# Performance work log

Hardware: AMD Instinct MI355X
Metric: run time of the kernel (lower is better)

## Reference

```python
import jax, jax.numpy as jnp
import numpy as np

N = 50000      # nodes
E = 800000     # edges (avg degree 16)
DIN = 256
DOUT = 256
EA = 16        # edge_attr_dim
EH = 32        # edge_mlp_hidden
Z = 0.8        # z_ratio
EPS = 1e-5


def _lin_init(k, fin, fout):
    k1, k2 = jax.random.split(k)
    s = 1.0 / np.sqrt(fin)
    W = jax.random.uniform(k1, (fin, fout), jnp.float32, -s, s)
    b = jax.random.uniform(k2, (fout,), jnp.float32, -s, s)
    return W, b


def setup_inputs() -> dict:
    key = jax.random.key(0)
    ks = jax.random.split(key, 12)
    x = jax.random.normal(ks[0], (N, DIN), dtype=jnp.float32)
    edge_index = jax.random.randint(ks[1], (2, E), 0, N, dtype=jnp.int64)
    edge_weight = jax.random.uniform(ks[2], (E,), dtype=jnp.float32)
    mask = jax.random.bernoulli(ks[3], 0.5, (N, 1))
    edge_attr = jax.random.normal(ks[4], (E, EA), dtype=jnp.float32)
    Wt0, bt0 = _lin_init(ks[5], DIN, DOUT)
    Wt1, bt1 = _lin_init(ks[6], DIN, DOUT)
    Wc0, bc0 = _lin_init(ks[7], DIN + DOUT, DOUT)
    Wc1, bc1 = _lin_init(ks[8], DIN + DOUT, DOUT)
    gn_w = jnp.ones((DOUT,), jnp.float32)
    gn_b = jnp.zeros((DOUT,), jnp.float32)
    gn_alpha = jnp.ones((DOUT,), jnp.float32)  # GraphNorm mean_scale
    Wm1, bm1 = _lin_init(ks[9], EA, EH)
    Wm2, bm2 = _lin_init(ks[10], EH, 1)
    return {
        'x': x, 'edge_index': edge_index, 'edge_weight': edge_weight,
        'mask': mask, 'edge_attr': edge_attr,
        'Wt0': Wt0, 'bt0': bt0, 'Wt1': Wt1, 'bt1': bt1,
        'Wc0': Wc0, 'bc0': bc0, 'Wc1': Wc1, 'bc1': bc1,
        'gn_w': gn_w, 'gn_b': gn_b, 'gn_alpha': gn_alpha,
        'Wm1': Wm1, 'bm1': bm1, 'Wm2': Wm2, 'bm2': bm2,
    }


def _mix(m, a1, a0):
    # torch.where(mask, z*x1 + (1-z)*x0, z*x0 + (1-z)*x1)
    return jnp.where(m, Z * a1 + (1.0 - Z) * a0, Z * a0 + (1.0 - Z) * a1)


def reference(x, edge_index, edge_weight, mask, edge_attr,
              Wt0, bt0, Wt1, bt1, Wc0, bc0, Wc1, bc1,
              gn_w, gn_b, gn_alpha, Wm1, bm1, Wm2, bm2):
    n_node = x.shape[0]
    row, col = edge_index[0], edge_index[1]

    # edge MLP (scalar mode): edge_weight <- softplus(MLP(edge_attr))
    h = jax.nn.relu(edge_attr @ Wm1 + bm1)
    ew = jax.nn.softplus((h @ Wm2 + bm2))[:, 0]  # [E]

    # buildAdj with aggr='mean': row-normalized weights
    deg = jax.ops.segment_sum(ew, row, num_segments=n_node)
    deg = jnp.where(deg < 0.5, deg + 1.0, deg)
    w = ew / deg[row]  # [E]

    # dual-branch transform + masked mix
    x1 = jax.nn.relu(x @ Wt1 + bt1)
    x0 = jax.nn.relu(x @ Wt0 + bt0)
    xm = _mix(mask, x1, x0)  # [N, DOUT]

    # sparse adj @ x : gather at col, scatter-add at row
    agg = jax.ops.segment_sum(w[:, None] * xm[col], row, num_segments=n_node)

    # GraphNorm (single graph): x - alpha*mean, normalize by std
    mean = jnp.mean(agg, axis=0)
    out = agg - gn_alpha * mean
    var = jnp.mean(out * out, axis=0)
    out = gn_w * out * jax.lax.rsqrt(var + EPS) + gn_b

    # dropout inactive in eval mode
    xc = jnp.concatenate([out, x], axis=-1)  # [N, DOUT+DIN]
    c1 = xc @ Wc1 + bc1
    c0 = xc @ Wc0 + bc0
    return _mix(mask, c1, c0)
```

## Files before the change

kernel.cpp:

```cpp
#include <hip/hip_runtime.h>

#define NN 50000
#define NE 800000
#define NNP 50176

typedef __attribute__((ext_vector_type(4))) float f32x4;
typedef __bf16 bf16x8 __attribute__((ext_vector_type(8)));

__device__ __forceinline__ float bfu2f(unsigned short u) {
  return __uint_as_float(((unsigned)u) << 16);
}
__device__ __forceinline__ unsigned short f2bf(float f) {
  unsigned u = __float_as_uint(f);
  u += 0x7fffu + ((u >> 16) & 1u);
  return (unsigned short)(u >> 16);
}

__global__ __launch_bounds__(256) void transpose_w(
    const float* __restrict__ W, unsigned short* __restrict__ WT, int K, int N) {
  __shared__ unsigned short T[32 * 40];
  const int t = threadIdx.x;
  const int k0 = blockIdx.x * 32, n0 = blockIdx.y * 32;
  const int kk = t >> 3, nn = (t & 7) * 4;
  f32x4 v = *(const f32x4*)(W + (k0 + kk) * N + n0 + nn);
#pragma unroll
  for (int i = 0; i < 4; i++) T[(nn + i) * 40 + kk] = f2bf(v[i]);
  __syncthreads();
  const int nn2 = t >> 3, kk2 = (t & 7) * 4;
  unsigned short o[4];
#pragma unroll
  for (int i = 0; i < 4; i++) o[i] = T[nn2 * 40 + kk2 + i];
  *(uint2*)(WT + (n0 + nn2) * K + k0 + kk2) = *(const uint2*)o;
}

__global__ __launch_bounds__(256) void count_kernel(
    const int* __restrict__ ei, int* __restrict__ cnt, int* __restrict__ rank) {
  const int e = blockIdx.x * 256 + threadIdx.x;
  if (e >= NE) return;
  rank[e] = atomicAdd(&cnt[ei[e]], 1);
}

__global__ __launch_bounds__(256) void scan1_kernel(const int* __restrict__ cnt,
                                                    int* __restrict__ blockSum) {
  __shared__ int sd[256];
  const int t = threadIdx.x;
  sd[t] = cnt[blockIdx.x * 256 + t];
  __syncthreads();
  for (int off = 128; off > 0; off >>= 1) {
    if (t < off) sd[t] += sd[t + off];
    __syncthreads();
  }
  if (t == 0) blockSum[blockIdx.x] = sd[0];
}

__global__ __launch_bounds__(256) void scan2_kernel(int* __restrict__ blockSum) {
  __shared__ int sd[256];
  const int t = threadIdx.x;
  int v = (t < 196) ? blockSum[t] : 0;
  sd[t] = v;
  __syncthreads();
  for (int off = 1; off < 256; off <<= 1) {
    int y = (t >= off) ? sd[t - off] : 0;
    __syncthreads();
    sd[t] += y;
    __syncthreads();
  }
  int ex = (t == 0) ? 0 : sd[t - 1];
  __syncthreads();
  if (t < 196) blockSum[t] = ex;
}

__global__ __launch_bounds__(256) void scan3_kernel(
    const int* __restrict__ cnt, const int* __restrict__ blockSum,
    int* __restrict__ start) {
  __shared__ int sd[256];
  const int t = threadIdx.x;
  const int row = blockIdx.x * 256 + t;
  const int c = cnt[row];
  sd[t] = c;
  __syncthreads();
  for (int off = 1; off < 256; off <<= 1) {
    int y = (t >= off) ? sd[t - off] : 0;
    __syncthreads();
    sd[t] += y;
    __syncthreads();
  }
  start[row] = blockSum[blockIdx.x] + sd[t] - c;
}

__device__ __forceinline__ void mlp4(float a0, float a1, float a2, float a3,
                                     const f32x4* __restrict__ w,
                                     f32x4& h0, f32x4& h1, f32x4& h2, f32x4& h3,
                                     f32x4& h4, f32x4& h5, f32x4& h6, f32x4& h7) {
  h0 += w[0] * a0;  h1 += w[1] * a0;  h2 += w[2] * a0;  h3 += w[3] * a0;
  h4 += w[4] * a0;  h5 += w[5] * a0;  h6 += w[6] * a0;  h7 += w[7] * a0;
  h0 += w[8] * a1;  h1 += w[9] * a1;  h2 += w[10] * a1; h3 += w[11] * a1;
  h4 += w[12] * a1; h5 += w[13] * a1; h6 += w[14] * a1; h7 += w[15] * a1;
  h0 += w[16] * a2; h1 += w[17] * a2; h2 += w[18] * a2; h3 += w[19] * a2;
  h4 += w[20] * a2; h5 += w[21] * a2; h6 += w[22] * a2; h7 += w[23] * a2;
  h0 += w[24] * a3; h1 += w[25] * a3; h2 += w[26] * a3; h3 += w[27] * a3;
  h4 += w[28] * a3; h5 += w[29] * a3; h6 += w[30] * a3; h7 += w[31] * a3;
}

__device__ __forceinline__ float rdot(f32x4 h, f32x4 w) {
  float s = fmaxf(h[0], 0.0f) * w[0];
  s = fmaf(fmaxf(h[1], 0.0f), w[1], s);
  s = fmaf(fmaxf(h[2], 0.0f), w[2], s);
  s = fmaf(fmaxf(h[3], 0.0f), w[3], s);
  return s;
}

__global__ __launch_bounds__(256) void mlp_fill_kernel(
    const float* __restrict__ ea,
    const float* __restrict__ Wm1, const float* __restrict__ bm1,
    const float* __restrict__ Wm2, const float* __restrict__ bm2,
    const int* __restrict__ ei, const int* __restrict__ start,
    const int* __restrict__ rank, uint2* __restrict__ colw) {
  __shared__ __align__(16) float w1[512];
  __shared__ __align__(16) float b1[32];
  __shared__ __align__(16) float w2[32];
  __shared__ float b2s[1];
  const int t = threadIdx.x;
  w1[t] = Wm1[t];
  w1[t + 256] = Wm1[t + 256];
  if (t < 32) { b1[t] = bm1[t]; w2[t] = Wm2[t]; }
  if (t == 0) b2s[0] = bm2[0];
  __syncthreads();
  const int e = blockIdx.x * 256 + t;
  if (e >= NE) return;
  f32x4 r0 = *(const f32x4*)(ea + e * 16);
  f32x4 r1 = *(const f32x4*)(ea + e * 16 + 4);
  f32x4 r2 = *(const f32x4*)(ea + e * 16 + 8);
  f32x4 r3 = *(const f32x4*)(ea + e * 16 + 12);
  const f32x4* bv = (const f32x4*)b1;
  f32x4 h0 = bv[0], h1 = bv[1], h2 = bv[2], h3 = bv[3];
  f32x4 h4 = bv[4], h5 = bv[5], h6 = bv[6], h7 = bv[7];
  const f32x4* wv = (const f32x4*)w1;
  mlp4(r0[0], r0[1], r0[2], r0[3], wv, h0, h1, h2, h3, h4, h5, h6, h7);
  mlp4(r1[0], r1[1], r1[2], r1[3], wv + 32, h0, h1, h2, h3, h4, h5, h6, h7);
  mlp4(r2[0], r2[1], r2[2], r2[3], wv + 64, h0, h1, h2, h3, h4, h5, h6, h7);
  mlp4(r3[0], r3[1], r3[2], r3[3], wv + 96, h0, h1, h2, h3, h4, h5, h6, h7);
  const f32x4* w2v = (const f32x4*)w2;
  float s = b2s[0];
  s += rdot(h0, w2v[0]) + rdot(h1, w2v[1]) + rdot(h2, w2v[2]) + rdot(h3, w2v[3]);
  s += rdot(h4, w2v[4]) + rdot(h5, w2v[5]) + rdot(h6, w2v[6]) + rdot(h7, w2v[7]);
  const float sp = (s > 0.0f) ? (s + log1pf(expf(-s))) : log1pf(expf(s));
  uint2 p;
  p.x = (unsigned)ei[NE + e];
  p.y = __float_as_uint(sp);
  colw[start[ei[e]] + rank[e]] = p;
}

__global__ __launch_bounds__(256, 2) void gemm_transform(
    const float* __restrict__ X,
    const unsigned short* __restrict__ WT1, const unsigned short* __restrict__ WT0,
    const float* __restrict__ bias1, const float* __restrict__ bias0,
    const int* __restrict__ mask, unsigned short* __restrict__ xmb) {
  __shared__ __align__(16) unsigned short As[128 * 40];
  __shared__ __align__(16) unsigned short Bs1[128 * 40];
  __shared__ __align__(16) unsigned short Bs0[128 * 40];
  const int t = threadIdx.x;
  const int col0 = blockIdx.x * 128, row0 = blockIdx.y * 128;
  const int wv = t >> 6, lane = t & 63, m = lane & 15, q = lane >> 4;
  const int hr = t >> 1, hc = t & 1;
  f32x4 acc1[2][8], acc0[2][8];
#pragma unroll
  for (int rf = 0; rf < 2; rf++)
#pragma unroll
    for (int nt = 0; nt < 8; nt++) { acc1[rf][nt] = (f32x4)(0.0f); acc0[rf][nt] = (f32x4)(0.0f); }
  const int gr = row0 + hr;
  for (int k0 = 0; k0 < 256; k0 += 32) {
    unsigned short av[16];
    if (gr < NN) {
      const float* xp = X + gr * 256 + k0 + hc * 16;
      f32x4 x0 = *(const f32x4*)(xp);
      f32x4 x1 = *(const f32x4*)(xp + 4);
      f32x4 x2 = *(const f32x4*)(xp + 8);
      f32x4 x3 = *(const f32x4*)(xp + 12);
#pragma unroll
      for (int i = 0; i < 4; i++) {
        av[i] = f2bf(x0[i]); av[4 + i] = f2bf(x1[i]);
        av[8 + i] = f2bf(x2[i]); av[12 + i] = f2bf(x3[i]);
      }
    } else {
#pragma unroll
      for (int i = 0; i < 16; i++) av[i] = 0;
    }
    *(uint4*)&As[hr * 40 + hc * 16] = ((const uint4*)av)[0];
    *(uint4*)&As[hr * 40 + hc * 16 + 8] = ((const uint4*)av)[1];
    const unsigned short* w1p = WT1 + (col0 + hr) * 256 + k0 + hc * 16;
    const unsigned short* w0p = WT0 + (col0 + hr) * 256 + k0 + hc * 16;
    uint4 b1a = *(const uint4*)w1p;
    uint4 b1b = *(const uint4*)(w1p + 8);
    uint4 b0a = *(const uint4*)w0p;
    uint4 b0b = *(const uint4*)(w0p + 8);
    *(uint4*)&Bs1[hr * 40 + hc * 16] = b1a;
    *(uint4*)&Bs1[hr * 40 + hc * 16 + 8] = b1b;
    *(uint4*)&Bs0[hr * 40 + hc * 16] = b0a;
    *(uint4*)&Bs0[hr * 40 + hc * 16 + 8] = b0b;
    __syncthreads();
    bf16x8 af[2];
#pragma unroll
    for (int rf = 0; rf < 2; rf++)
      af[rf] = *(const bf16x8*)&As[(wv * 32 + rf * 16 + m) * 40 + q * 8];
#pragma unroll
    for (int nt = 0; nt < 8; nt++) {
      bf16x8 f1 = *(const bf16x8*)&Bs1[(nt * 16 + m) * 40 + q * 8];
      bf16x8 f0 = *(const bf16x8*)&Bs0[(nt * 16 + m) * 40 + q * 8];
      acc1[0][nt] = __builtin_amdgcn_mfma_f32_16x16x32_bf16(af[0], f1, acc1[0][nt], 0, 0, 0);
      acc1[1][nt] = __builtin_amdgcn_mfma_f32_16x16x32_bf16(af[1], f1, acc1[1][nt], 0, 0, 0);
      acc0[0][nt] = __builtin_amdgcn_mfma_f32_16x16x32_bf16(af[0], f0, acc0[0][nt], 0, 0, 0);
      acc0[1][nt] = __builtin_amdgcn_mfma_f32_16x16x32_bf16(af[1], f0, acc0[1][nt], 0, 0, 0);
    }
    __syncthreads();
  }
#pragma unroll
  for (int rf = 0; rf < 2; rf++) {
    const int rbase = row0 + wv * 32 + rf * 16 + q * 4;
    int mk[4];
#pragma unroll
    for (int r = 0; r < 4; r++) mk[r] = (rbase + r < NN) ? mask[rbase + r] : 0;
#pragma unroll
    for (int nt = 0; nt < 8; nt++) {
      const int gc = col0 + nt * 16 + m;
      const float bb1 = bias1[gc];
      const float bb0 = bias0[gc];
#pragma unroll
      for (int r = 0; r < 4; r++) {
        const int grr = rbase + r;
        if (grr < NN) {
          float v1 = fmaxf(acc1[rf][nt][r] + bb1, 0.0f);
          float v0 = fmaxf(acc0[rf][nt][r] + bb0, 0.0f);
          float o = mk[r] ? (0.8f * v1 + 0.2f * v0) : (0.8f * v0 + 0.2f * v1);
          xmb[grr * 256 + gc] = f2bf(o);
        }
      }
    }
  }
}

__global__ __launch_bounds__(256) void aggregate_kernel(
    const int* __restrict__ start, const int* __restrict__ cnt,
    const uint2* __restrict__ colw,
    const unsigned short* __restrict__ xmb, unsigned short* __restrict__ aggb) {
  const int wave = threadIdx.x >> 6, lane = threadIdx.x & 63;
  const int row = blockIdx.x * 4 + wave;
  const int s = start[row];
  const int c = cnt[row];
  const int choff = lane * 4;
  f32x4 acc = (f32x4)(0.0f);
  float dsum = 0.0f;
  int i = 0;
  for (; i + 4 <= c; i += 4) {
    uint2 cw0 = colw[s + i], cw1 = colw[s + i + 1];
    uint2 cw2 = colw[s + i + 2], cw3 = colw[s + i + 3];
    const float w0 = __uint_as_float(cw0.y), w1 = __uint_as_float(cw1.y);
    const float w2 = __uint_as_float(cw2.y), w3 = __uint_as_float(cw3.y);
    uint2 u0 = *(const uint2*)(xmb + (int)cw0.x * 256 + choff);
    uint2 u1 = *(const uint2*)(xmb + (int)cw1.x * 256 + choff);
    uint2 u2 = *(const uint2*)(xmb + (int)cw2.x * 256 + choff);
    uint2 u3 = *(const uint2*)(xmb + (int)cw3.x * 256 + choff);
    dsum += (w0 + w1) + (w2 + w3);
    acc[0] = fmaf(w0, __uint_as_float(u0.x << 16), acc[0]);
    acc[1] = fmaf(w0, __uint_as_float(u0.x & 0xffff0000u), acc[1]);
    acc[2] = fmaf(w0, __uint_as_float(u0.y << 16), acc[2]);
    acc[3] = fmaf(w0, __uint_as_float(u0.y & 0xffff0000u), acc[3]);
    acc[0] = fmaf(w1, __uint_as_float(u1.x << 16), acc[0]);
    acc[1] = fmaf(w1, __uint_as_float(u1.x & 0xffff0000u), acc[1]);
    acc[2] = fmaf(w1, __uint_as_float(u1.y << 16), acc[2]);
    acc[3] = fmaf(w1, __uint_as_float(u1.y & 0xffff0000u), acc[3]);
    acc[0] = fmaf(w2, __uint_as_float(u2.x << 16), acc[0]);
    acc[1] = fmaf(w2, __uint_as_float(u2.x & 0xffff0000u), acc[1]);
    acc[2] = fmaf(w2, __uint_as_float(u2.y << 16), acc[2]);
    acc[3] = fmaf(w2, __uint_as_float(u2.y & 0xffff0000u), acc[3]);
    acc[0] = fmaf(w3, __uint_as_float(u3.x << 16), acc[0]);
    acc[1] = fmaf(w3, __uint_as_float(u3.x & 0xffff0000u), acc[1]);
    acc[2] = fmaf(w3, __uint_as_float(u3.y << 16), acc[2]);
    acc[3] = fmaf(w3, __uint_as_float(u3.y & 0xffff0000u), acc[3]);
  }
  for (; i < c; i++) {
    uint2 cw0 = colw[s + i];
    const float w0 = __uint_as_float(cw0.y);
    uint2 u0 = *(const uint2*)(xmb + (int)cw0.x * 256 + choff);
    dsum += w0;
    acc[0] = fmaf(w0, __uint_as_float(u0.x << 16), acc[0]);
    acc[1] = fmaf(w0, __uint_as_float(u0.x & 0xffff0000u), acc[1]);
    acc[2] = fmaf(w0, __uint_as_float(u0.y << 16), acc[2]);
    acc[3] = fmaf(w0, __uint_as_float(u0.y & 0xffff0000u), acc[3]);
  }
  float d = (dsum < 0.5f) ? dsum + 1.0f : dsum;
  const float inv = 1.0f / d;
  unsigned short o[4];
#pragma unroll
  for (int j = 0; j < 4; j++) o[j] = f2bf(acc[j] * inv);
  *(uint2*)(aggb + row * 256 + choff) = *(const uint2*)o;
}

__global__ __launch_bounds__(256) void stats_kernel(
    const unsigned short* __restrict__ aggb, float* __restrict__ S1, float* __restrict__ S2) {
  const int c = threadIdx.x;
  const int r0 = blockIdx.x * 200;
  float s1 = 0.0f, s2 = 0.0f;
  for (int r = 0; r < 200; r++) {
    float v = bfu2f(aggb[(r0 + r) * 256 + c]);
    s1 += v;
    s2 = fmaf(v, v, s2);
  }
  unsafeAtomicAdd(&S1[c], s1);
  unsafeAtomicAdd(&S2[c], s2);
}

__global__ void finalize_kernel(
    const float* __restrict__ S1, const float* __restrict__ S2,
    const float* __restrict__ gw, const float* __restrict__ gb,
    const float* __restrict__ ga,
    float* __restrict__ scale, float* __restrict__ shift) {
  const int c = threadIdx.x;
  const float inv_n = 1.0f / (float)NN;
  float mean = S1[c] * inv_n;
  float ex2 = S2[c] * inv_n;
  float am = ga[c] * mean;
  float var = ex2 - 2.0f * am * mean + am * am;
  float sc = gw[c] * rsqrtf(var + 1e-5f);
  scale[c] = sc;
  shift[c] = gb[c] - sc * am;
}

__global__ __launch_bounds__(256, 2) void gemm_combine(
    const unsigned short* __restrict__ aggb,
    const float* __restrict__ scale, const float* __restrict__ shift,
    const float* __restrict__ X,
    const unsigned short* __restrict__ WT1, const unsigned short* __restrict__ WT0,
    const float* __restrict__ bias1, const float* __restrict__ bias0,
    const int* __restrict__ mask, float* __restrict__ out) {
  __shared__ __align__(16) unsigned short As[128 * 40];
  __shared__ __align__(16) unsigned short Bs1[128 * 40];
  __shared__ __align__(16) unsigned short Bs0[128 * 40];
  __shared__ float scL[256];
  __shared__ float shL[256];
  const int t = threadIdx.x;
  scL[t] = scale[t];
  shL[t] = shift[t];
  const int col0 = blockIdx.x * 128, row0 = blockIdx.y * 128;
  const int wv = t >> 6, lane = t & 63, m = lane & 15, q = lane >> 4;
  const int hr = t >> 1, hc = t & 1;
  f32x4 acc1[2][8], acc0[2][8];
#pragma unroll
  for (int rf = 0; rf < 2; rf++)
#pragma unroll
    for (int nt = 0; nt < 8; nt++) { acc1[rf][nt] = (f32x4)(0.0f); acc0[rf][nt] = (f32x4)(0.0f); }
  const int gr = row0 + hr;
  __syncthreads();
  for (int k0 = 0; k0 < 512; k0 += 32) {
    unsigned short av[16];
#pragma unroll
    for (int i = 0; i < 16; i++) av[i] = 0;
    if (gr < NN) {
      if (k0 < 256) {
        const int c0 = k0 + hc * 16;
        uint4 ua = *(const uint4*)(aggb + gr * 256 + c0);
        uint4 ub = *(const uint4*)(aggb + gr * 256 + c0 + 8);
        const unsigned short* us = (const unsigned short*)&ua;
        const unsigned short* vs = (const unsigned short*)&ub;
#pragma unroll
        for (int i = 0; i < 8; i++) {
          av[i] = f2bf(fmaf(scL[c0 + i], bfu2f(us[i]), shL[c0 + i]));
          av[8 + i] = f2bf(fmaf(scL[c0 + 8 + i], bfu2f(vs[i]), shL[c0 + 8 + i]));
        }
      } else {
        const float* xp = X + gr * 256 + (k0 - 256) + hc * 16;
        f32x4 x0 = *(const f32x4*)(xp);
        f32x4 x1 = *(const f32x4*)(xp + 4);
        f32x4 x2 = *(const f32x4*)(xp + 8);
        f32x4 x3 = *(const f32x4*)(xp + 12);
#pragma unroll
        for (int i = 0; i < 4; i++) {
          av[i] = f2bf(x0[i]); av[4 + i] = f2bf(x1[i]);
          av[8 + i] = f2bf(x2[i]); av[12 + i] = f2bf(x3[i]);
        }
      }
    }
    *(uint4*)&As[hr * 40 + hc * 16] = ((const uint4*)av)[0];
    *(uint4*)&As[hr * 40 + hc * 16 + 8] = ((const uint4*)av)[1];
    const unsigned short* w1p = WT1 + (col0 + hr) * 512 + k0 + hc * 16;
    const unsigned short* w0p = WT0 + (col0 + hr) * 512 + k0 + hc * 16;
    uint4 b1a = *(const uint4*)w1p;
    uint4 b1b = *(const uint4*)(w1p + 8);
    uint4 b0a = *(const uint4*)w0p;
    uint4 b0b = *(const uint4*)(w0p + 8);
    *(uint4*)&Bs1[hr * 40 + hc * 16] = b1a;
    *(uint4*)&Bs1[hr * 40 + hc * 16 + 8] = b1b;
    *(uint4*)&Bs0[hr * 40 + hc * 16] = b0a;
    *(uint4*)&Bs0[hr * 40 + hc * 16 + 8] = b0b;
    __syncthreads();
    bf16x8 af[2];
#pragma unroll
    for (int rf = 0; rf < 2; rf++)
      af[rf] = *(const bf16x8*)&As[(wv * 32 + rf * 16 + m) * 40 + q * 8];
#pragma unroll
    for (int nt = 0; nt < 8; nt++) {
      bf16x8 f1 = *(const bf16x8*)&Bs1[(nt * 16 + m) * 40 + q * 8];
      bf16x8 f0 = *(const bf16x8*)&Bs0[(nt * 16 + m) * 40 + q * 8];
      acc1[0][nt] = __builtin_amdgcn_mfma_f32_16x16x32_bf16(af[0], f1, acc1[0][nt], 0, 0, 0);
      acc1[1][nt] = __builtin_amdgcn_mfma_f32_16x16x32_bf16(af[1], f1, acc1[1][nt], 0, 0, 0);
      acc0[0][nt] = __builtin_amdgcn_mfma_f32_16x16x32_bf16(af[0], f0, acc0[0][nt], 0, 0, 0);
      acc0[1][nt] = __builtin_amdgcn_mfma_f32_16x16x32_bf16(af[1], f0, acc0[1][nt], 0, 0, 0);
    }
    __syncthreads();
  }
#pragma unroll
  for (int rf = 0; rf < 2; rf++) {
    const int rbase = row0 + wv * 32 + rf * 16 + q * 4;
    int mk[4];
#pragma unroll
    for (int r = 0; r < 4; r++) mk[r] = (rbase + r < NN) ? mask[rbase + r] : 0;
#pragma unroll
    for (int nt = 0; nt < 8; nt++) {
      const int gc = col0 + nt * 16 + m;
      const float bb1 = bias1[gc];
      const float bb0 = bias0[gc];
#pragma unroll
      for (int r = 0; r < 4; r++) {
        const int grr = rbase + r;
        if (grr < NN) {
          float v1 = acc1[rf][nt][r] + bb1;
          float v0 = acc0[rf][nt][r] + bb0;
          float o = mk[r] ? (0.8f * v1 + 0.2f * v0) : (0.8f * v0 + 0.2f * v1);
          out[grr * 256 + gc] = o;
        }
      }
    }
  }
}

extern "C" void kernel_launch(void* const* d_in, const int* in_sizes, int n_in,
                              void* d_out, int out_size, void* d_ws, size_t ws_size,
                              hipStream_t stream) {
  (void)in_sizes; (void)n_in; (void)out_size; (void)ws_size;
  const float* x   = (const float*)d_in[0];
  const int*   ei  = (const int*)d_in[1];
  const int*   msk = (const int*)d_in[3];
  const float* ea  = (const float*)d_in[4];
  const float* Wt0 = (const float*)d_in[5];
  const float* bt0 = (const float*)d_in[6];
  const float* Wt1 = (const float*)d_in[7];
  const float* bt1 = (const float*)d_in[8];
  const float* Wc0 = (const float*)d_in[9];
  const float* bc0 = (const float*)d_in[10];
  const float* Wc1 = (const float*)d_in[11];
  const float* bc1 = (const float*)d_in[12];
  const float* gnw = (const float*)d_in[13];
  const float* gnb = (const float*)d_in[14];
  const float* gna = (const float*)d_in[15];
  const float* Wm1 = (const float*)d_in[16];
  const float* bm1 = (const float*)d_in[17];
  const float* Wm2 = (const float*)d_in[18];
  const float* bm2 = (const float*)d_in[19];

  char* ws = (char*)d_ws;
  int* cnt      = (int*)ws;
  int* startA   = (int*)(ws + 200704);
  int* blockSum = (int*)(ws + 401408);
  float* S1     = (float*)(ws + 402432);
  float* S2     = (float*)(ws + 402432 + 1024);
  float* scaleP = (float*)(ws + 402432 + 2048);
  float* shiftP = (float*)(ws + 402432 + 3072);
  int* rankA    = (int*)(ws + 1048576);
  uint2* colw   = (uint2*)(ws + 4248576);
  unsigned short* xmb  = (unsigned short*)(ws + 10648576);
  unsigned short* aggb = (unsigned short*)(ws + 36248576);
  unsigned short* WTt1 = (unsigned short*)(ws + 61848576);
  unsigned short* WTt0 = (unsigned short*)(ws + 61979648);
  unsigned short* WTc1 = (unsigned short*)(ws + 62110720);
  unsigned short* WTc0 = (unsigned short*)(ws + 62372864);

  hipMemsetAsync(ws, 0, 406528, stream);

  transpose_w<<<dim3(8, 8), 256, 0, stream>>>(Wt1, WTt1, 256, 256);
  transpose_w<<<dim3(8, 8), 256, 0, stream>>>(Wt0, WTt0, 256, 256);
  transpose_w<<<dim3(16, 8), 256, 0, stream>>>(Wc1, WTc1, 512, 256);
  transpose_w<<<dim3(16, 8), 256, 0, stream>>>(Wc0, WTc0, 512, 256);

  count_kernel<<<3125, 256, 0, stream>>>(ei, cnt, rankA);
  scan1_kernel<<<196, 256, 0, stream>>>(cnt, blockSum);
  scan2_kernel<<<1, 256, 0, stream>>>(blockSum);
  scan3_kernel<<<196, 256, 0, stream>>>(cnt, blockSum, startA);
  mlp_fill_kernel<<<3125, 256, 0, stream>>>(ea, Wm1, bm1, Wm2, bm2, ei, startA, rankA, colw);
  gemm_transform<<<dim3(2, 391), 256, 0, stream>>>(x, WTt1, WTt0, bt1, bt0, msk, xmb);
  aggregate_kernel<<<12500, 256, 0, stream>>>(startA, cnt, colw, xmb, aggb);
  stats_kernel<<<250, 256, 0, stream>>>(aggb, S1, S2);
  finalize_kernel<<<1, 256, 0, stream>>>(S1, S2, gnw, gnb, gna, scaleP, shiftP);
  gemm_combine<<<dim3(2, 391), 256, 0, stream>>>(aggb, scaleP, shiftP, x, WTc1, WTc0,
                                                 bc1, bc0, msk, (float*)d_out);
}
```

Before: 441.4 us.

## Pre-convert inputs to bf16 and unify GEMMs with async LDS loads

Converts x to bf16 once in a separate kernel, and folds the GraphNorm finalize into a kernel that writes normalized bf16 aggregates, reusing the xmb buffer. Both GEMMs become one templated kernel that loads A and B tiles straight into LDS with global_load_lds and an XOR swizzle. The new kernel uses 128x64 tiles with K=64 steps, a block-index swizzle for cache locality, and a launch bound allowing 3 blocks per SIMD. This removes the per-tile fp32-to-bf16 conversion and the normalization math from the GEMM inner loops, at the cost of extra full-size passes over memory for the conversion and normalization kernels.

```diff
diff --git a/kernel.cpp b/kernel.cpp
--- a/kernel.cpp
+++ b/kernel.cpp
@@ -16,6 +16,12 @@
   return (unsigned short)(u >> 16);
 }
 
+__device__ __forceinline__ void gload16(const void* g, void* l) {
+  __builtin_amdgcn_global_load_lds(
+      (const __attribute__((address_space(1))) unsigned int*)g,
+      (__attribute__((address_space(3))) unsigned int*)l, 16, 0, 0);
+}
+
 __global__ __launch_bounds__(256) void transpose_w(
     const float* __restrict__ W, unsigned short* __restrict__ WT, int K, int N) {
   __shared__ unsigned short T[32 * 40];
@@ -31,6 +37,24 @@
 #pragma unroll
   for (int i = 0; i < 4; i++) o[i] = T[nn2 * 40 + kk2 + i];
   *(uint2*)(WT + (n0 + nn2) * K + k0 + kk2) = *(const uint2*)o;
+}
+
+__global__ __launch_bounds__(256) void x2bf_kernel(
+    const float* __restrict__ X, unsigned short* __restrict__ xbf) {
+  const int gid = blockIdx.x * 256 + threadIdx.x;
+  const long base = (long)gid * 8;
+  const int row = (int)(base >> 8);
+  unsigned short o[8];
+  if (row < NN) {
+    f32x4 a = *(const f32x4*)(X + base);
+    f32x4 b = *(const f32x4*)(X + base + 4);
+#pragma unroll
+    for (int i = 0; i < 4; i++) { o[i] = f2bf(a[i]); o[4 + i] = f2bf(b[i]); }
+  } else {
+#pragma unroll
+    for (int i = 0; i < 8; i++) o[i] = 0;
+  }
+  *(uint4*)(xbf + base) = *(const uint4*)o;
 }
 
 __global__ __launch_bounds__(256) void count_kernel(
@@ -151,88 +175,99 @@
   colw[start[ei[e]] + rank[e]] = p;
 }
 
-__global__ __launch_bounds__(256, 2) void gemm_transform(
-    const float* __restrict__ X,
+template <int KTOT, bool SPLIT, bool OUT_BF16>
+__global__ __launch_bounds__(256, 3) void gemm_dual(
+    const unsigned short* __restrict__ A0, const unsigned short* __restrict__ A1,
     const unsigned short* __restrict__ WT1, const unsigned short* __restrict__ WT0,
     const float* __restrict__ bias1, const float* __restrict__ bias0,
-    const int* __restrict__ mask, unsigned short* __restrict__ xmb) {
-  __shared__ __align__(16) unsigned short As[128 * 40];
-  __shared__ __align__(16) unsigned short Bs1[128 * 40];
-  __shared__ __align__(16) unsigned short Bs0[128 * 40];
-  const int t = threadIdx.x;
-  const int col0 = blockIdx.x * 128, row0 = blockIdx.y * 128;
+    const int* __restrict__ mask, void* __restrict__ outp) {
+  __shared__ __align__(16) unsigned short Al[128 * 64];
+  __shared__ __align__(16) unsigned short B1l[64 * 64];
+  __shared__ __align__(16) unsigned short B0l[64 * 64];
+  const int t = threadIdx.x;
+  const int bid = blockIdx.y * gridDim.x + blockIdx.x;
+  const int swz = (bid & 7) * 196 + (bid >> 3);
+  const int bx = swz & 3, by = swz >> 2;
+  const int row0 = by * 128, col0 = bx * 64;
   const int wv = t >> 6, lane = t & 63, m = lane & 15, q = lane >> 4;
-  const int hr = t >> 1, hc = t & 1;
-  f32x4 acc1[2][8], acc0[2][8];
-#pragma unroll
-  for (int rf = 0; rf < 2; rf++)
-#pragma unroll
-    for (int nt = 0; nt < 8; nt++) { acc1[rf][nt] = (f32x4)(0.0f); acc0[rf][nt] = (f32x4)(0.0f); }
-  const int gr = row0 + hr;
-  for (int k0 = 0; k0 < 256; k0 += 32) {
-    unsigned short av[16];
-    if (gr < NN) {
-      const float* xp = X + gr * 256 + k0 + hc * 16;
-      f32x4 x0 = *(const f32x4*)(xp);
-      f32x4 x1 = *(const f32x4*)(xp + 4);
-      f32x4 x2 = *(const f32x4*)(xp + 8);
-      f32x4 x3 = *(const f32x4*)(xp + 12);
-#pragma unroll
-      for (int i = 0; i < 4; i++) {
-        av[i] = f2bf(x0[i]); av[4 + i] = f2bf(x1[i]);
-        av[8 + i] = f2bf(x2[i]); av[12 + i] = f2bf(x3[i]);
+  const int wr = wv >> 1, wc = wv & 1;
+  const int arow = t >> 3, ach = t & 7;
+  f32x4 acc1[4][2], acc0[4][2];
+#pragma unroll
+  for (int rf = 0; rf < 4; rf++)
+#pragma unroll
+    for (int nt = 0; nt < 2; nt++) { acc1[rf][nt] = (f32x4)(0.0f); acc0[rf][nt] = (f32x4)(0.0f); }
+
+  for (int k0 = 0; k0 < KTOT; k0 += 64) {
+    const unsigned short* Ab;
+    int kr;
+    if constexpr (SPLIT) {
+      if (k0 < 256) { Ab = A0; kr = k0; } else { Ab = A1; kr = k0 - 256; }
+    } else { Ab = A0; kr = k0; }
+#pragma unroll
+    for (int i = 0; i < 4; i++) {
+      const int r = arow + i * 32;
+      gload16(Ab + (size_t)(row0 + r) * 256 + kr + ((ach ^ (r & 7)) << 3),
+              &Al[(i * 256 + t) * 8]);
+    }
+#pragma unroll
+    for (int i = 0; i < 2; i++) {
+      const int r = arow + i * 32;
+      const int sc = (ach ^ (r & 7)) << 3;
+      gload16(WT1 + (size_t)(col0 + r) * KTOT + k0 + sc, &B1l[(i * 256 + t) * 8]);
+      gload16(WT0 + (size_t)(col0 + r) * KTOT + k0 + sc, &B0l[(i * 256 + t) * 8]);
+    }
+    __syncthreads();
+#pragma unroll
+    for (int kk = 0; kk < 2; kk++) {
+      bf16x8 af[4];
+#pragma unroll
+      for (int rf = 0; rf < 4; rf++) {
+        const int r = wr * 64 + rf * 16 + m;
+        af[rf] = *(const bf16x8*)&Al[r * 64 + (((kk * 4 + q) ^ (r & 7)) << 3)];
       }
-    } else {
-#pragma unroll
-      for (int i = 0; i < 16; i++) av[i] = 0;
+#pragma unroll
+      for (int nt = 0; nt < 2; nt++) {
+        const int n = wc * 32 + nt * 16 + m;
+        const int off = n * 64 + (((kk * 4 + q) ^ (n & 7)) << 3);
+        bf16x8 f1 = *(const bf16x8*)&B1l[off];
+        bf16x8 f0 = *(const bf16x8*)&B0l[off];
+#pragma unroll
+        for (int rf = 0; rf < 4; rf++) {
+          acc1[rf][nt] = __builtin_amdgcn_mfma_f32_16x16x32_bf16(af[rf], f1, acc1[rf][nt], 0, 0, 0);
+          acc0[rf][nt] = __builtin_amdgcn_mfma_f32_16x16x32_bf16(af[rf], f0, acc0[rf][nt], 0, 0, 0);
+        }
+      }
     }
-    *(uint4*)&As[hr * 40 + hc * 16] = ((const uint4*)av)[0];
-    *(uint4*)&As[hr * 40 + hc * 16 + 8] = ((const uint4*)av)[1];
-    const unsigned short* w1p = WT1 + (col0 + hr) * 256 + k0 + hc * 16;
-    const unsigned short* w0p = WT0 + (col0 + hr) * 256 + k0 + hc * 16;
-    uint4 b1a = *(const uint4*)w1p;
-    uint4 b1b = *(const uint4*)(w1p + 8);
-    uint4 b0a = *(const uint4*)w0p;
-    uint4 b0b = *(const uint4*)(w0p + 8);
-    *(uint4*)&Bs1[hr * 40 + hc * 16] = b1a;
-    *(uint4*)&Bs1[hr * 40 + hc * 16 + 8] = b1b;
-    *(uint4*)&Bs0[hr * 40 + hc * 16] = b0a;
-    *(uint4*)&Bs0[hr * 40 + hc * 16 + 8] = b0b;
-    __syncthreads();
-    bf16x8 af[2];
-#pragma unroll
-    for (int rf = 0; rf < 2; rf++)
-      af[rf] = *(const bf16x8*)&As[(wv * 32 + rf * 16 + m) * 40 + q * 8];
-#pragma unroll
-    for (int nt = 0; nt < 8; nt++) {
-      bf16x8 f1 = *(const bf16x8*)&Bs1[(nt * 16 + m) * 40 + q * 8];
-      bf16x8 f0 = *(const bf16x8*)&Bs0[(nt * 16 + m) * 40 + q * 8];
-      acc1[0][nt] = __builtin_amdgcn_mfma_f32_16x16x32_bf16(af[0], f1, acc1[0][nt], 0, 0, 0);
-      acc1[1][nt] = __builtin_amdgcn_mfma_f32_16x16x32_bf16(af[1], f1, acc1[1][nt], 0, 0, 0);
-      acc0[0][nt] = __builtin_amdgcn_mfma_f32_16x16x32_bf16(af[0], f0, acc0[0][nt], 0, 0, 0);
-      acc0[1][nt] = __builtin_amdgcn_mfma_f32_16x16x32_bf16(af[1], f0, acc0[1][nt], 0, 0, 0);
-    }
-    __syncthreads();
-  }
-#pragma unroll
-  for (int rf = 0; rf < 2; rf++) {
-    const int rbase = row0 + wv * 32 + rf * 16 + q * 4;
+    __syncthreads();
+  }
+
+#pragma unroll
+  for (int rf = 0; rf < 4; rf++) {
+    const int rbase = row0 + wr * 64 + rf * 16 + q * 4;
     int mk[4];
 #pragma unroll
     for (int r = 0; r < 4; r++) mk[r] = (rbase + r < NN) ? mask[rbase + r] : 0;
 #pragma unroll
-    for (int nt = 0; nt < 8; nt++) {
-      const int gc = col0 + nt * 16 + m;
+    for (int nt = 0; nt < 2; nt++) {
+      const int gc = col0 + wc * 32 + nt * 16 + m;
       const float bb1 = bias1[gc];
       const float bb0 = bias0[gc];
 #pragma unroll
       for (int r = 0; r < 4; r++) {
         const int grr = rbase + r;
         if (grr < NN) {
-          float v1 = fmaxf(acc1[rf][nt][r] + bb1, 0.0f);
-          float v0 = fmaxf(acc0[rf][nt][r] + bb0, 0.0f);
-          float o = mk[r] ? (0.8f * v1 + 0.2f * v0) : (0.8f * v0 + 0.2f * v1);
-          xmb[grr * 256 + gc] = f2bf(o);
+          float v1 = acc1[rf][nt][r] + bb1;
+          float v0 = acc0[rf][nt][r] + bb0;
+          if constexpr (OUT_BF16) {
+            v1 = fmaxf(v1, 0.0f);
+            v0 = fmaxf(v0, 0.0f);
+            float o = mk[r] ? (0.8f * v1 + 0.2f * v0) : (0.8f * v0 + 0.2f * v1);
+            ((unsigned short*)outp)[(size_t)grr * 256 + gc] = f2bf(o);
+          } else {
+            float o = mk[r] ? (0.8f * v1 + 0.2f * v0) : (0.8f * v0 + 0.2f * v1);
+            ((float*)outp)[(size_t)grr * 256 + gc] = o;
+          }
         }
       }
     }
@@ -310,127 +345,40 @@
   unsafeAtomicAdd(&S2[c], s2);
 }
 
-__global__ void finalize_kernel(
+__global__ __launch_bounds__(256) void norm_agg_kernel(
+    const unsigned short* __restrict__ aggb,
     const float* __restrict__ S1, const float* __restrict__ S2,
     const float* __restrict__ gw, const float* __restrict__ gb,
-    const float* __restrict__ ga,
-    float* __restrict__ scale, float* __restrict__ shift) {
-  const int c = threadIdx.x;
-  const float inv_n = 1.0f / (float)NN;
-  float mean = S1[c] * inv_n;
-  float ex2 = S2[c] * inv_n;
-  float am = ga[c] * mean;
-  float var = ex2 - 2.0f * am * mean + am * am;
-  float sc = gw[c] * rsqrtf(var + 1e-5f);
-  scale[c] = sc;
-  shift[c] = gb[c] - sc * am;
-}
-
-__global__ __launch_bounds__(256, 2) void gemm_combine(
-    const unsigned short* __restrict__ aggb,
-    const float* __restrict__ scale, const float* __restrict__ shift,
-    const float* __restrict__ X,
-    const unsigned short* __restrict__ WT1, const unsigned short* __restrict__ WT0,
-    const float* __restrict__ bias1, const float* __restrict__ bias0,
-    const int* __restrict__ mask, float* __restrict__ out) {
-  __shared__ __align__(16) unsigned short As[128 * 40];
-  __shared__ __align__(16) unsigned short Bs1[128 * 40];
-  __shared__ __align__(16) unsigned short Bs0[128 * 40];
+    const float* __restrict__ ga, unsigned short* __restrict__ aggn) {
   __shared__ float scL[256];
   __shared__ float shL[256];
   const int t = threadIdx.x;
-  scL[t] = scale[t];
-  shL[t] = shift[t];
-  const int col0 = blockIdx.x * 128, row0 = blockIdx.y * 128;
-  const int wv = t >> 6, lane = t & 63, m = lane & 15, q = lane >> 4;
-  const int hr = t >> 1, hc = t & 1;
-  f32x4 acc1[2][8], acc0[2][8];
-#pragma unroll
-  for (int rf = 0; rf < 2; rf++)
-#pragma unroll
-    for (int nt = 0; nt < 8; nt++) { acc1[rf][nt] = (f32x4)(0.0f); acc0[rf][nt] = (f32x4)(0.0f); }
-  const int gr = row0 + hr;
-  __syncthreads();
-  for (int k0 = 0; k0 < 512; k0 += 32) {
-    unsigned short av[16];
-#pragma unroll
-    for (int i = 0; i < 16; i++) av[i] = 0;
-    if (gr < NN) {
-      if (k0 < 256) {
-        const int c0 = k0 + hc * 16;
-        uint4 ua = *(const uint4*)(aggb + gr * 256 + c0);
-        uint4 ub = *(const uint4*)(aggb + gr * 256 + c0 + 8);
-        const unsigned short* us = (const unsigned short*)&ua;
-        const unsigned short* vs = (const unsigned short*)&ub;
-#pragma unroll
-        for (int i = 0; i < 8; i++) {
-          av[i] = f2bf(fmaf(scL[c0 + i], bfu2f(us[i]), shL[c0 + i]));
-          av[8 + i] = f2bf(fmaf(scL[c0 + 8 + i], bfu2f(vs[i]), shL[c0 + 8 + i]));
-        }
-      } else {
-        const float* xp = X + gr * 256 + (k0 - 256) + hc * 16;
-        f32x4 x0 = *(const f32x4*)(xp);
-        f32x4 x1 = *(const f32x4*)(xp + 4);
-        f32x4 x2 = *(const f32x4*)(xp + 8);
-        f32x4 x3 = *(const f32x4*)(xp + 12);
-#pragma unroll
-        for (int i = 0; i < 4; i++) {
-          av[i] = f2bf(x0[i]); av[4 + i] = f2bf(x1[i]);
-          av[8 + i] = f2bf(x2[i]); av[12 + i] = f2bf(x3[i]);
-        }
-      }
-    }
-    *(uint4*)&As[hr * 40 + hc * 16] = ((const uint4*)av)[0];
-    *(uint4*)&As[hr * 40 + hc * 16 + 8] = ((const uint4*)av)[1];
-    const unsigned short* w1p = WT1 + (col0 + hr) * 512 + k0 + hc * 16;
-    const unsigned short* w0p = WT0 + (col0 + hr) * 512 + k0 + hc * 16;
-    uint4 b1a = *(const uint4*)w1p;
-    uint4 b1b = *(const uint4*)(w1p + 8);
-    uint4 b0a = *(const uint4*)w0p;
-    uint4 b0b = *(const uint4*)(w0p + 8);
-    *(uint4*)&Bs1[hr * 40 + hc * 16] = b1a;
-    *(uint4*)&Bs1[hr * 40 + hc * 16 + 8] = b1b;
-    *(uint4*)&Bs0[hr * 40 + hc * 16] = b0a;
-    *(uint4*)&Bs0[hr * 40 + hc * 16 + 8] = b0b;
-    __syncthreads();
-    bf16x8 af[2];
-#pragma unroll
-    for (int rf = 0; rf < 2; rf++)
-      af[rf] = *(const bf16x8*)&As[(wv * 32 + rf * 16 + m) * 40 + q * 8];
-#pragma unroll
-    for (int nt = 0; nt < 8; nt++) {
-      bf16x8 f1 = *(const bf16x8*)&Bs1[(nt * 16 + m) * 40 + q * 8];
-      bf16x8 f0 = *(const bf16x8*)&Bs0[(nt * 16 + m) * 40 + q * 8];
-      acc1[0][nt] = __builtin_amdgcn_mfma_f32_16x16x32_bf16(af[0], f1, acc1[0][nt], 0, 0, 0);
-      acc1[1][nt] = __builtin_amdgcn_mfma_f32_16x16x32_bf16(af[1], f1, acc1[1][nt], 0, 0, 0);
-      acc0[0][nt] = __builtin_amdgcn_mfma_f32_16x16x32_bf16(af[0], f0, acc0[0][nt], 0, 0, 0);
-      acc0[1][nt] = __builtin_amdgcn_mfma_f32_16x16x32_bf16(af[1], f0, acc0[1][nt], 0, 0, 0);
-    }
-    __syncthreads();
-  }
-#pragma unroll
-  for (int rf = 0; rf < 2; rf++) {
-    const int rbase = row0 + wv * 32 + rf * 16 + q * 4;
-    int mk[4];
-#pragma unroll
-    for (int r = 0; r < 4; r++) mk[r] = (rbase + r < NN) ? mask[rbase + r] : 0;
-#pragma unroll
-    for (int nt = 0; nt < 8; nt++) {
-      const int gc = col0 + nt * 16 + m;
-      const float bb1 = bias1[gc];
-      const float bb0 = bias0[gc];
-#pragma unroll
-      for (int r = 0; r < 4; r++) {
-        const int grr = rbase + r;
-        if (grr < NN) {
-          float v1 = acc1[rf][nt][r] + bb1;
-          float v0 = acc0[rf][nt][r] + bb0;
-          float o = mk[r] ? (0.8f * v1 + 0.2f * v0) : (0.8f * v0 + 0.2f * v1);
-          out[grr * 256 + gc] = o;
-        }
-      }
-    }
-  }
+  {
+    const float inv_n = 1.0f / (float)NN;
+    float mean = S1[t] * inv_n;
+    float ex2 = S2[t] * inv_n;
+    float am = ga[t] * mean;
+    float var = ex2 - 2.0f * am * mean + am * am;
+    float sc = gw[t] * rsqrtf(var + 1e-5f);
+    scL[t] = sc;
+    shL[t] = gb[t] - sc * am;
+  }
+  __syncthreads();
+  const int gid = blockIdx.x * 256 + t;
+  const long base = (long)gid * 8;
+  const int row = (int)(base >> 8);
+  const int c = (int)(base & 255);
+  unsigned short o[8];
+  if (row < NN) {
+    uint4 u = *(const uint4*)(aggb + base);
+    const unsigned short* us = (const unsigned short*)&u;
+#pragma unroll
+    for (int i = 0; i < 8; i++) o[i] = f2bf(fmaf(scL[c + i], bfu2f(us[i]), shL[c + i]));
+  } else {
+#pragma unroll
+    for (int i = 0; i < 8; i++) o[i] = 0;
+  }
+  *(uint4*)(aggn + base) = *(const uint4*)o;
 }
 
 extern "C" void kernel_launch(void* const* d_in, const int* in_sizes, int n_in,
@@ -462,34 +410,38 @@
   int* startA   = (int*)(ws + 200704);
   int* blockSum = (int*)(ws + 401408);
   float* S1     = (float*)(ws + 402432);
-  float* S2     = (float*)(ws + 402432 + 1024);
-  float* scaleP = (float*)(ws + 402432 + 2048);
-  float* shiftP = (float*)(ws + 402432 + 3072);
-  int* rankA    = (int*)(ws + 1048576);
-  uint2* colw   = (uint2*)(ws + 4248576);
-  unsigned short* xmb  = (unsigned short*)(ws + 10648576);
-  unsigned short* aggb = (unsigned short*)(ws + 36248576);
-  unsigned short* WTt1 = (unsigned short*)(ws + 61848576);
-  unsigned short* WTt0 = (unsigned short*)(ws + 61979648);
-  unsigned short* WTc1 = (unsigned short*)(ws + 62110720);
-  unsigned short* WTc0 = (unsigned short*)(ws + 62372864);
-
-  hipMemsetAsync(ws, 0, 406528, stream);
+  float* S2     = (float*)(ws + 403456);
+  unsigned short* WTt1 = (unsigned short*)(ws + 404480);
+  unsigned short* WTt0 = (unsigned short*)(ws + 535552);
+  unsigned short* WTc1 = (unsigned short*)(ws + 666624);
+  unsigned short* WTc0 = (unsigned short*)(ws + 928768);
+  int* rankA    = (int*)(ws + 1190912);
+  uint2* colw   = (uint2*)(ws + 4390912);
+  unsigned short* xmb  = (unsigned short*)(ws + 10790912);
+  unsigned short* aggb = (unsigned short*)(ws + 36481024);
+  unsigned short* xbf  = (unsigned short*)(ws + 62171136);
+
+  hipMemsetAsync(ws, 0, 404480, stream);
 
   transpose_w<<<dim3(8, 8), 256, 0, stream>>>(Wt1, WTt1, 256, 256);
   transpose_w<<<dim3(8, 8), 256, 0, stream>>>(Wt0, WTt0, 256, 256);
   transpose_w<<<dim3(16, 8), 256, 0, stream>>>(Wc1, WTc1, 512, 256);
   transpose_w<<<dim3(16, 8), 256, 0, stream>>>(Wc0, WTc0, 512, 256);
+  x2bf_kernel<<<6272, 256, 0, stream>>>(x, xbf);
 
   count_kernel<<<3125, 256, 0, stream>>>(ei, cnt, rankA);
   scan1_kernel<<<196, 256, 0, stream>>>(cnt, blockSum);
   scan2_kernel<<<1, 256, 0, stream>>>(blockSum);
   scan3_kernel<<<196, 256, 0, stream>>>(cnt, blockSum, startA);
   mlp_fill_kernel<<<3125, 256, 0, stream>>>(ea, Wm1, bm1, Wm2, bm2, ei, startA, rankA, colw);
-  gemm_transform<<<dim3(2, 391), 256, 0, stream>>>(x, WTt1, WTt0, bt1, bt0, msk, xmb);
+
+  gemm_dual<256, false, true><<<dim3(4, 392), 256, 0, stream>>>(
+      xbf, (const unsigned short*)nullptr, WTt1, WTt0, bt1, bt0, msk, xmb);
+
   aggregate_kernel<<<12500, 256, 0, stream>>>(startA, cnt, colw, xmb, aggb);
   stats_kernel<<<250, 256, 0, stream>>>(aggb, S1, S2);
-  finalize_kernel<<<1, 256, 0, stream>>>(S1, S2, gnw, gnb, gna, scaleP, shiftP);
-  gemm_combine<<<dim3(2, 391), 256, 0, stream>>>(aggb, scaleP, shiftP, x, WTc1, WTc0,
-                                                 bc1, bc0, msk, (float*)d_out);
-}
+  norm_agg_kernel<<<6272, 256, 0, stream>>>(aggb, S1, S2, gnw, gnb, gna, xmb );
+
+  gemm_dual<512, true, false><<<dim3(4, 392), 256, 0, stream>>>(
+      xmb , xbf, WTc1, WTc0, bc1, bc0, msk, d_out);
+}
```

Result: faster. 403.8 us (-8.5%).
